# Kernel optimization log

Measured on AMD Instinct MI355X. Metric: run time of the kernel, lower is better.

Reference implementation:

```python
import jax, jax.numpy as jnp
import numpy as np

H = 16      # num_attention_heads
D = 64      # attention_head_size
HID = H * D # hidden_size = 1024
N = 1024    # seq_len == max_len
K = 1024    # position_buckets == att_span (K >= N so un-clamped indices stay in range)
EPS = 1e-7  # layer_norm_eps


def setup_inputs() -> dict:
    key = jax.random.key(0)
    ks = jax.random.split(key, 12)

    def w(k, shape):
        return jax.random.normal(k, shape, dtype=jnp.float32) * 0.02

    return {
        "hidden_states": jax.random.normal(ks[0], (1, N, HID), dtype=jnp.float32),
        "rel_embeddings": jax.random.normal(ks[1], (2 * K, HID), dtype=jnp.float32),
        "Wq": w(ks[2], (HID, HID)), "bq": jnp.zeros((HID,), jnp.float32),
        "Wk": w(ks[3], (HID, HID)), "bk": jnp.zeros((HID,), jnp.float32),
        "Wv": w(ks[4], (HID, HID)), "bv": jnp.zeros((HID,), jnp.float32),
        "Wpk": w(ks[5], (HID, HID)), "bpk": jnp.zeros((HID,), jnp.float32),
        "Wpq": w(ks[6], (HID, HID)), "bpq": jnp.zeros((HID,), jnp.float32),
        "Wo": w(ks[7], (HID, HID)), "bo": jnp.zeros((HID,), jnp.float32),
        "ln_g": jnp.ones((HID,), jnp.float32),
        "ln_b": jnp.zeros((HID,), jnp.float32),
    }


def _heads(x):
    # (L, HID) -> (H, L, D)   (batch size is 1, matching the baked-in id offsets)
    L = x.shape[0]
    return x.reshape(L, H, D).transpose(1, 0, 2)


def reference(hidden_states, rel_embeddings, Wq, bq, Wk, bk, Wv, bv,
              Wpk, bpk, Wpq, bpq, Wo, bo, ln_g, ln_b):
    hs = hidden_states[0]                       # (N, HID)
    q = _heads(hs @ Wq.T + bq)                  # (H, N, D)
    k = _heads(hs @ Wk.T + bk)                  # (H, N, D)
    v = _heads(hs @ Wv.T + bv)                  # (H, N, D)

    scale = jnp.sqrt(jnp.asarray(D * 3, jnp.float32))  # scale_factor = 1 + c2p + p2c = 3
    scores = jnp.einsum('hid,hjd->hij', q, k) / scale  # (H, N, N)

    pos_k = _heads(rel_embeddings @ Wpk.T + bpk)       # (H, 2K, D)
    pos_q = _heads(rel_embeddings @ Wpq.T + bpq)       # (H, 2K, D)

    rows = jnp.arange(N)[:, None]                      # (N, 1)
    # ids[i, j] = (i - j) + K  (no clamp in the original; valid since K >= N)
    idx = K + jnp.arange(N)[:, None] - jnp.arange(N)[None, :]  # (N, N)

    # c2p: gather c2p_att[h, i, K + i - j]
    c2p_att = jnp.einsum('hid,hkd->hik', q, pos_k)     # (H, N, 2K)
    c2p = c2p_att[:, rows, idx]                        # (H, N, N)

    # p2c: gather p2c_att[h, i, K + j - i], then transpose last two dims
    p2c_att = jnp.einsum('hid,hkd->hik', k, pos_q)     # (H, N, 2K)
    p2c = jnp.swapaxes(p2c_att[:, rows, idx.T], -1, -2)  # (H, N, N)

    scores = scores + (c2p + p2c) / scale
    attn = jax.nn.softmax(scores, axis=-1)             # (H, N, N)

    ctx = jnp.einsum('hij,hjd->hid', attn, v)          # (H, N, D)
    ctx = ctx.transpose(1, 0, 2).reshape(1, N, HID)    # (1, N, HID)

    # DebertaV2SelfOutput: dense + residual LayerNorm
    out = ctx @ Wo.T + bo
    x = out + hidden_states
    mu = jnp.mean(x, axis=-1, keepdims=True)
    var = jnp.mean(jnp.square(x - mu), axis=-1, keepdims=True)
    return ((x - mu) / jnp.sqrt(var + EPS)) * ln_g + ln_b
```

## Files before the change

### kernel.cpp

```cpp
#include <hip/hip_runtime.h>
#include <stdint.h>

#define HID 1024
#define NSEQ 1024
#define KREL 1024
#define NHEAD 16
#define DHEAD 64

typedef __attribute__((ext_vector_type(8))) short bhalf8;
typedef __attribute__((ext_vector_type(4))) float floatx4;

__device__ inline uint16_t f2bf(float f) {
  union { float f; uint32_t u; } c; c.f = f;
  uint32_t u = c.u;
  return (uint16_t)((u + 0x7fffu + ((u >> 16) & 1u)) >> 16);
}
__device__ inline uint32_t pkbf(float a, float b) {
  union { float f; uint32_t u; } x, y; x.f = a; y.f = b;
#if __has_builtin(__builtin_amdgcn_perm)
  return __builtin_amdgcn_perm(x.u + 0x8000u, y.u + 0x8000u, 0x03020706u);
#else
  return ((x.u + 0x8000u) >> 16) | ((y.u + 0x8000u) & 0xffff0000u);
#endif
}

struct Cast8 {
  const float* src[8];
  uint16_t* dst[8];
  int n[8];
};
__global__ __launch_bounds__(256) void cast8_kernel(Cast8 c) {
  int seg = blockIdx.y;
  int n = c.n[seg];
  const float* s = c.src[seg];
  uint16_t* d = c.dst[seg];
  for (int idx = (blockIdx.x * 256 + threadIdx.x) * 4; idx < n; idx += 1024 * 256 * 4) {
    float4 v = *(const float4*)(s + idx);
    ushort4 o;
    o.x = f2bf(v.x); o.y = f2bf(v.y); o.z = f2bf(v.z); o.w = f2bf(v.w);
    *(ushort4*)(d + idx) = o;
  }
}

struct ProjArgs {
  const uint16_t* A[5];
  const uint16_t* W[5];
  const float* bias[5];
  uint16_t* C[5];
  int trans[5];
};
__global__ __launch_bounds__(256) void proj_gemm(ProjArgs pa) {
  __shared__ uint16_t a_s[2][128 * 40];
  __shared__ uint16_t b_s[2][128 * 40];
  int bidx = blockIdx.x;
  int xcd = bidx & 7, idx = bidx >> 3;
  int g = xcd * 7 + (idx >> 3);
  int nt = idx & 7;
  int z, mt;
  if (g < 24) { z = g >> 3; mt = g & 7; }
  else { int g2 = g - 24; z = 3 + (g2 >> 4); mt = g2 & 15; }
  const uint16_t* A = pa.A[z];
  const uint16_t* W = pa.W[z];
  int i0 = mt * 128, n0 = nt * 128;

  int t = threadIdx.x;
  int lane = t & 63, w = t >> 6;
  int fm = lane & 15, kq = lane >> 4;
  int wm = (w >> 1) * 64, wn = (w & 1) * 64;

  int ra = t >> 1, ca = (t & 1) * 16;
  const uint16_t* Ap = A + (size_t)(i0 + ra) * HID + ca;
  const uint16_t* Wp = W + (size_t)(n0 + ra) * HID + ca;

  floatx4 acc[4][4] = {};

  uint4 ua0 = *(const uint4*)(Ap);
  uint4 ua1 = *(const uint4*)(Ap + 8);
  uint4 ub0 = *(const uint4*)(Wp);
  uint4 ub1 = *(const uint4*)(Wp + 8);
  *(uint4*)(&a_s[0][ra * 40 + ca]) = ua0;
  *(uint4*)(&a_s[0][ra * 40 + ca + 8]) = ua1;
  *(uint4*)(&b_s[0][ra * 40 + ca]) = ub0;
  *(uint4*)(&b_s[0][ra * 40 + ca + 8]) = ub1;

  for (int kt = 0; kt < 32; ++kt) {
    __syncthreads();
    int cur = kt & 1;
    if (kt < 31) {
      int ko = (kt + 1) * 32;
      ua0 = *(const uint4*)(Ap + ko);
      ua1 = *(const uint4*)(Ap + ko + 8);
      ub0 = *(const uint4*)(Wp + ko);
      ub1 = *(const uint4*)(Wp + ko + 8);
    }
    const uint16_t* as = &a_s[cur][0];
    const uint16_t* bs = &b_s[cur][0];
    bhalf8 af[4], bf[4];
#pragma unroll
    for (int m2 = 0; m2 < 4; ++m2)
      af[m2] = *(bhalf8*)(as + (wm + m2 * 16 + fm) * 40 + kq * 8);
#pragma unroll
    for (int n2 = 0; n2 < 4; ++n2)
      bf[n2] = *(bhalf8*)(bs + (wn + n2 * 16 + fm) * 40 + kq * 8);
#pragma unroll
    for (int m2 = 0; m2 < 4; ++m2)
#pragma unroll
      for (int n2 = 0; n2 < 4; ++n2)
        acc[m2][n2] = __builtin_amdgcn_mfma_f32_16x16x32_bf16(af[m2], bf[n2], acc[m2][n2], 0, 0, 0);
    if (kt < 31) {
      int nxt = cur ^ 1;
      *(uint4*)(&a_s[nxt][ra * 40 + ca]) = ua0;
      *(uint4*)(&a_s[nxt][ra * 40 + ca + 8]) = ua1;
      *(uint4*)(&b_s[nxt][ra * 40 + ca]) = ub0;
      *(uint4*)(&b_s[nxt][ra * 40 + ca + 8]) = ub1;
    }
  }

  const float* bias = pa.bias[z];
  uint16_t* C = pa.C[z];
  int tr = pa.trans[z];
#pragma unroll
  for (int m2 = 0; m2 < 4; ++m2) {
    int rowb = i0 + wm + m2 * 16 + kq * 4;
#pragma unroll
    for (int n2 = 0; n2 < 4; ++n2) {
      int col = n0 + wn + n2 * 16 + fm;
      float bv = bias[col];
      floatx4 v = acc[m2][n2];
      if (tr) {
        uint2 p = { pkbf(v[0] + bv, v[1] + bv), pkbf(v[2] + bv, v[3] + bv) };
        *(uint2*)(C + (size_t)col * NSEQ + rowb) = p;
      } else {
#pragma unroll
        for (int r = 0; r < 4; ++r)
          C[(size_t)(rowb + r) * HID + col] = f2bf(v[r] + bv);
      }
    }
  }
}

__global__ __launch_bounds__(256) void out_gemm(const uint16_t* __restrict__ Abf,
                                                const uint16_t* __restrict__ W,
                                                const float* __restrict__ bias,
                                                float* __restrict__ C) {
  __shared__ uint16_t a_s[2][64 * 40];
  __shared__ uint16_t b_s[2][64 * 40];
  int bidx = blockIdx.x;
  int i0 = (bidx >> 4) * 64, n0 = (bidx & 15) * 64;
  int t = threadIdx.x;
  int lane = t & 63, w = t >> 6;
  int fm = lane & 15, kq = lane >> 4;
  int wm = (w >> 1) * 32, wn = (w & 1) * 32;
  int ra = t >> 2, ca = (t & 3) * 8;
  const uint16_t* Ap = Abf + (size_t)(i0 + ra) * HID + ca;
  const uint16_t* Wp = W + (size_t)(n0 + ra) * HID + ca;
  floatx4 acc00 = {0,0,0,0}, acc01 = {0,0,0,0}, acc10 = {0,0,0,0}, acc11 = {0,0,0,0};
  uint4 ua = *(const uint4*)(Ap);
  uint4 ub = *(const uint4*)(Wp);
  *(uint4*)(&a_s[0][ra * 40 + ca]) = ua;
  *(uint4*)(&b_s[0][ra * 40 + ca]) = ub;
  for (int kt = 0; kt < 32; ++kt) {
    __syncthreads();
    int cur = kt & 1;
    if (kt < 31) {
      int ko = (kt + 1) * 32;
      ua = *(const uint4*)(Ap + ko);
      ub = *(const uint4*)(Wp + ko);
    }
    const uint16_t* as = &a_s[cur][0];
    const uint16_t* bs = &b_s[cur][0];
    bhalf8 a0 = *(bhalf8*)(as + (wm + fm) * 40 + kq * 8);
    bhalf8 a1 = *(bhalf8*)(as + (wm + 16 + fm) * 40 + kq * 8);
    bhalf8 b0 = *(bhalf8*)(bs + (wn + fm) * 40 + kq * 8);
    bhalf8 b1 = *(bhalf8*)(bs + (wn + 16 + fm) * 40 + kq * 8);
    acc00 = __builtin_amdgcn_mfma_f32_16x16x32_bf16(a0, b0, acc00, 0, 0, 0);
    acc01 = __builtin_amdgcn_mfma_f32_16x16x32_bf16(a0, b1, acc01, 0, 0, 0);
    acc10 = __builtin_amdgcn_mfma_f32_16x16x32_bf16(a1, b0, acc10, 0, 0, 0);
    acc11 = __builtin_amdgcn_mfma_f32_16x16x32_bf16(a1, b1, acc11, 0, 0, 0);
    if (kt < 31) {
      int nxt = cur ^ 1;
      *(uint4*)(&a_s[nxt][ra * 40 + ca]) = ua;
      *(uint4*)(&b_s[nxt][ra * 40 + ca]) = ub;
    }
  }
  int rb0 = kq * 4;
#define EPO(ACC, SM, SN)                                                   \
  {                                                                        \
    int rowb = i0 + wm + (SM)*16 + rb0;                                    \
    int col = n0 + wn + (SN)*16 + fm;                                      \
    float bv_ = bias[col];                                                 \
    _Pragma("unroll")                                                      \
    for (int rr = 0; rr < 4; ++rr)                                         \
      C[(size_t)(rowb + rr) * HID + col] = ACC[rr] + bv_;                  \
  }
  EPO(acc00, 0, 0) EPO(acc01, 0, 1) EPO(acc10, 1, 0) EPO(acc11, 1, 1)
#undef EPO
}

__global__ __launch_bounds__(256) void attn_kernel(const uint16_t* __restrict__ qg,
                                                   const uint16_t* __restrict__ kg,
                                                   const uint16_t* __restrict__ vtg,
                                                   const uint16_t* __restrict__ pkg,
                                                   const uint16_t* __restrict__ pqg,
                                                   uint16_t* __restrict__ ctx) {
  const float RSCALE = 0.07216878364870323f;
  __shared__ uint16_t Qs[32][72];
  __shared__ uint16_t Ks[32][72];
  __shared__ uint16_t Vt[64][40];
  __shared__ float C2Ps[2][32][68];
  __shared__ float P2C[2][32][68];
  __shared__ float Sqk[2][32][36];
  __shared__ uint16_t Pbf[32][40];
  __shared__ float m_sm[32], l_sm[32], al_sm[32];

  int t = threadIdx.x;
  int lane = t & 63, w = t >> 6;
  int fm = lane & 15;
  int kq = lane >> 4;

  int b = blockIdx.x;
  int xcd = b & 7, slot = b >> 3;
  int h = xcd * 2 + (slot & 1);
  int i0 = (slot >> 1) * 32;
  int cb = h * DHEAD;

  {
    int r = t >> 3, chq = (t & 7) * 8;
    *(uint4*)(&Qs[r][chq]) = *(const uint4*)(qg + (size_t)(i0 + r) * HID + cb + chq);
  }
  if (t < 32) { m_sm[t] = -1e30f; l_sm[t] = 0.f; }

  floatx4 opv0 = {0,0,0,0}, opv1 = {0,0,0,0};
  int wn = w * 16;
  int smt = w >> 1, snt = w & 1;
  int i2 = t >> 3, jj4 = (t & 7) * 4;

  int pr = t >> 3, pch = (t & 7) * 8;
  int rV = t >> 2, cV = (t & 3) * 8;
  const uint16_t* kb = kg + cb + pch;
  const uint16_t* vb = vtg + (size_t)(cb + rV) * HID + cV;

  int ntb = (w & 1) * 2;
  int brow_f = ntb * 16 + fm;
  const uint16_t* bgp = ((w < 2) ? pkg : pqg) + cb + kq * 8;
  int cbase = 31 - brow_f + kq * 4;

  uint4 rk, rv;
  bhalf8 nbA0, nbA1, nbB0, nbB1;

#define STAGE1(BUF, BA0, BA1, BB0, BB1)                                          \
  do {                                                                           \
    if (w < 2) {                                                                 \
      _Pragma("unroll")                                                          \
      for (int mt = 0; mt < 2; ++mt) {                                           \
        bhalf8 a0 = *(bhalf8*)(&Qs[mt * 16 + fm][kq * 8]);                       \
        bhalf8 a1 = *(bhalf8*)(&Qs[mt * 16 + fm][kq * 8 + 32]);                  \
        floatx4 ac0 = {0,0,0,0}, ac1 = {0,0,0,0};                                \
        ac0 = __builtin_amdgcn_mfma_f32_16x16x32_bf16(a0, BA0, ac0, 0, 0, 0);    \
        ac0 = __builtin_amdgcn_mfma_f32_16x16x32_bf16(a1, BA1, ac0, 0, 0, 0);    \
        ac1 = __builtin_amdgcn_mfma_f32_16x16x32_bf16(a0, BB0, ac1, 0, 0, 0);    \
        ac1 = __builtin_amdgcn_mfma_f32_16x16x32_bf16(a1, BB1, ac1, 0, 0, 0);    \
        _Pragma("unroll")                                                        \
        for (int r = 0; r < 4; ++r) {                                            \
          int i = mt * 16 + kq * 4 + r;                                          \
          C2Ps[BUF][i][(cbase + mt * 16 + r) & 63] = ac0[r];                     \
          C2Ps[BUF][i][(cbase + mt * 16 + r - 16) & 63] = ac1[r];                \
        }                                                                        \
      }                                                                          \
    } else {                                                                     \
      _Pragma("unroll")                                                          \
      for (int mt = 0; mt < 2; ++mt) {                                           \
        bhalf8 a0 = *(bhalf8*)(&Ks[mt * 16 + fm][kq * 8]);                       \
        bhalf8 a1 = *(bhalf8*)(&Ks[mt * 16 + fm][kq * 8 + 32]);                  \
        floatx4 ac0 = {0,0,0,0}, ac1 = {0,0,0,0};                                \
        ac0 = __builtin_amdgcn_mfma_f32_16x16x32_bf16(a0, BA0, ac0, 0, 0, 0);    \
        ac0 = __builtin_amdgcn_mfma_f32_16x16x32_bf16(a1, BA1, ac0, 0, 0, 0);    \
        ac1 = __builtin_amdgcn_mfma_f32_16x16x32_bf16(a0, BB0, ac1, 0, 0, 0);    \
        ac1 = __builtin_amdgcn_mfma_f32_16x16x32_bf16(a1, BB1, ac1, 0, 0, 0);    \
        _Pragma("unroll")                                                        \
        for (int r = 0; r < 4; ++r) {                                            \
          int jr = mt * 16 + kq * 4 + r;                                         \
          P2C[BUF][jr][brow_f] = ac0[r];                                         \
          P2C[BUF][jr][brow_f + 16] = ac1[r];                                    \
        }                                                                        \
      }                                                                          \
    }                                                                            \
    {                                                                            \
      bhalf8 qa0 = *(bhalf8*)(&Qs[smt * 16 + fm][kq * 8]);                       \
      bhalf8 qa1 = *(bhalf8*)(&Qs[smt * 16 + fm][kq * 8 + 32]);                  \
      bhalf8 kb0 = *(bhalf8*)(&Ks[snt * 16 + fm][kq * 8]);                       \
      bhalf8 kb1 = *(bhalf8*)(&Ks[snt * 16 + fm][kq * 8 + 32]);                  \
      floatx4 sacc = {0,0,0,0};                                                  \
      sacc = __builtin_amdgcn_mfma_f32_16x16x32_bf16(qa0, kb0, sacc, 0, 0, 0);   \
      sacc = __builtin_amdgcn_mfma_f32_16x16x32_bf16(qa1, kb1, sacc, 0, 0, 0);   \
      _Pragma("unroll")                                                          \
      for (int r = 0; r < 4; ++r)                                                \
        Sqk[BUF][smt * 16 + kq * 4 + r][snt * 16 + fm] = sacc[r];                \
    }                                                                            \
  } while (0)

  rk = *(const uint4*)(kb);
  rv = *(const uint4*)(vb);
  *(uint4*)(&Ks[pr][pch]) = rk;
  *(uint4*)(&Vt[rV][cV]) = rv;
  __syncthreads();
  rk = *(const uint4*)(kb + (size_t)(32 + pr) * HID);
  rv = *(const uint4*)(vb + 32);
  {
    int rbase = KREL + i0 - 31;
    int r0 = rbase + brow_f;      if (r0 > 2047) r0 = 2047;
    int r1 = rbase + brow_f + 16; if (r1 > 2047) r1 = 2047;
    bhalf8 tA0 = *(const bhalf8*)(bgp + ((size_t)r0 << 10));
    bhalf8 tA1 = *(const bhalf8*)(bgp + ((size_t)r0 << 10) + 32);
    bhalf8 tB0 = *(const bhalf8*)(bgp + ((size_t)r1 << 10));
    bhalf8 tB1 = *(const bhalf8*)(bgp + ((size_t)r1 << 10) + 32);
    STAGE1(0, tA0, tA1, tB0, tB1);
  }
  __syncthreads();
  {
    *(uint4*)(&Ks[pr][pch]) = rk;
    rk = *(const uint4*)(kb + (size_t)(64 + pr) * HID);
    int rb1 = KREL + i0 - 63;
    int r0 = rb1 + brow_f;
    nbA0 = *(const bhalf8*)(bgp + ((size_t)r0 << 10));
    nbA1 = *(const bhalf8*)(bgp + ((size_t)r0 << 10) + 32);
    nbB0 = *(const bhalf8*)(bgp + ((size_t)(r0 + 16) << 10));
    nbB1 = *(const bhalf8*)(bgp + ((size_t)(r0 + 16) << 10) + 32);
  }
  __syncthreads();

  for (int jt = 0; jt < NSEQ / 32; ++jt) {
    int cur = jt & 1;

    float4 v_sqk = *(const float4*)(&Sqk[cur][i2][jj4]);
    float4 v_c2p = *(const float4*)(&C2Ps[cur][i2][jj4]);
    float p0 = P2C[cur][jj4 + 0][i2 - jj4 + 31];
    float p1 = P2C[cur][jj4 + 1][i2 - jj4 + 30];
    float p2 = P2C[cur][jj4 + 2][i2 - jj4 + 29];
    float p3 = P2C[cur][jj4 + 3][i2 - jj4 + 28];

    if (jt < 31) {
      int bi = cur ^ 1;
      STAGE1(bi, nbA0, nbA1, nbB0, nbB1);
    }

    {
      float sv0 = (v_sqk.x + v_c2p.x + p0) * RSCALE;
      float sv1 = (v_sqk.y + v_c2p.y + p1) * RSCALE;
      float sv2 = (v_sqk.z + v_c2p.z + p2) * RSCALE;
      float sv3 = (v_sqk.w + v_c2p.w + p3) * RSCALE;
      float mx = fmaxf(fmaxf(sv0, sv1), fmaxf(sv2, sv3));
      mx = fmaxf(mx, __shfl_xor(mx, 1));
      mx = fmaxf(mx, __shfl_xor(mx, 2));
      mx = fmaxf(mx, __shfl_xor(mx, 4));
      float m_old = m_sm[i2];
      float m_new = fmaxf(m_old, mx);
      float al = __expf(m_old - m_new);
      float e0 = __expf(sv0 - m_new);
      float e1 = __expf(sv1 - m_new);
      float e2 = __expf(sv2 - m_new);
      float e3 = __expf(sv3 - m_new);
      uint2 pk2v;
      pk2v.x = (uint32_t)f2bf(e0) | ((uint32_t)f2bf(e1) << 16);
      pk2v.y = (uint32_t)f2bf(e2) | ((uint32_t)f2bf(e3) << 16);
      *(uint2*)(&Pbf[i2][jj4]) = pk2v;
      float ts = (e0 + e1) + (e2 + e3);
      ts += __shfl_xor(ts, 1);
      ts += __shfl_xor(ts, 2);
      ts += __shfl_xor(ts, 4);
      if (jj4 == 0) { m_sm[i2] = m_new; l_sm[i2] = l_sm[i2] * al + ts; al_sm[i2] = al; }
    }
    __syncthreads();

    {
      floatx4 al0 = *(const floatx4*)(&al_sm[kq * 4]);
      floatx4 al1 = *(const floatx4*)(&al_sm[16 + kq * 4]);
#pragma unroll
      for (int r = 0; r < 4; ++r) {
        opv0[r] *= al0[r];
        opv1[r] *= al1[r];
      }
      bhalf8 vbf = *(bhalf8*)(&Vt[wn + fm][kq * 8]);
      bhalf8 pa0 = *(bhalf8*)(&Pbf[fm][kq * 8]);
      bhalf8 pa1 = *(bhalf8*)(&Pbf[16 + fm][kq * 8]);
      opv0 = __builtin_amdgcn_mfma_f32_16x16x32_bf16(pa0, vbf, opv0, 0, 0, 0);
      opv1 = __builtin_amdgcn_mfma_f32_16x16x32_bf16(pa1, vbf, opv1, 0, 0, 0);
      if (jt < 31) *(uint4*)(&Vt[rV][cV]) = rv;
      if (jt < 30) rv = *(const uint4*)(vb + (jt + 2) * 32);
    }
    if (jt < 30) {
      *(uint4*)(&Ks[pr][pch]) = rk;
    }
    if (jt < 29) {
      rk = *(const uint4*)(kb + (size_t)((jt + 3) * 32 + pr) * HID);
    }
    if (jt < 30) {
      int rb = KREL + i0 - (jt + 2) * 32 - 31;
      int r0 = rb + brow_f;
      nbA0 = *(const bhalf8*)(bgp + ((size_t)r0 << 10));
      nbA1 = *(const bhalf8*)(bgp + ((size_t)r0 << 10) + 32);
      nbB0 = *(const bhalf8*)(bgp + ((size_t)(r0 + 16) << 10));
      nbB1 = *(const bhalf8*)(bgp + ((size_t)(r0 + 16) << 10) + 32);
    }
    __syncthreads();
  }
#undef STAGE1

  {
    floatx4 l0 = *(const floatx4*)(&l_sm[kq * 4]);
    floatx4 l1 = *(const floatx4*)(&l_sm[16 + kq * 4]);
#pragma unroll
    for (int r = 0; r < 4; ++r) {
      int ia = kq * 4 + r, ib = 16 + kq * 4 + r;
      ctx[(size_t)(i0 + ia) * HID + cb + wn + fm] = f2bf(opv0[r] / l0[r]);
      ctx[(size_t)(i0 + ib) * HID + cb + wn + fm] = f2bf(opv1[r] / l1[r]);
    }
  }
}

__global__ __launch_bounds__(256) void ln_kernel(const float* __restrict__ xin,
                                                 const float* __restrict__ hs,
                                                 const float* __restrict__ g,
                                                 const float* __restrict__ b,
                                                 float* __restrict__ y) {
  int row = blockIdx.x, t = threadIdx.x;
  int c = t * 4;
  float4 a = *(const float4*)(xin + (size_t)row * HID + c);
  float4 hv = *(const float4*)(hs + (size_t)row * HID + c);
  float x0 = a.x + hv.x, x1 = a.y + hv.y, x2 = a.z + hv.z, x3 = a.w + hv.w;
  float s = x0 + x1 + x2 + x3;
  float sq = x0 * x0 + x1 * x1 + x2 * x2 + x3 * x3;
  for (int off = 32; off; off >>= 1) {
    s += __shfl_xor(s, off);
    sq += __shfl_xor(sq, off);
  }
  __shared__ float rs[4], rq[4];
  int w = t >> 6, lane = t & 63;
  if (lane == 0) { rs[w] = s; rq[w] = sq; }
  __syncthreads();
  s = rs[0] + rs[1] + rs[2] + rs[3];
  sq = rq[0] + rq[1] + rq[2] + rq[3];
  float mu = s * (1.0f / HID);
  float var = sq * (1.0f / HID) - mu * mu;
  float rstd = rsqrtf(var + 1e-7f);
  float4 gg = *(const float4*)(g + c);
  float4 bb = *(const float4*)(b + c);
  float4 out;
  out.x = (x0 - mu) * rstd * gg.x + bb.x;
  out.y = (x1 - mu) * rstd * gg.y + bb.y;
  out.z = (x2 - mu) * rstd * gg.z + bb.z;
  out.w = (x3 - mu) * rstd * gg.w + bb.w;
  *(float4*)(y + (size_t)row * HID + c) = out;
}

extern "C" void kernel_launch(void* const* d_in, const int* in_sizes, int n_in,
                              void* d_out, int out_size, void* d_ws, size_t ws_size,
                              hipStream_t stream) {
  const float* hs  = (const float*)d_in[0];
  const float* rel = (const float*)d_in[1];
  const float* Wq  = (const float*)d_in[2];  const float* bq  = (const float*)d_in[3];
  const float* Wk  = (const float*)d_in[4];  const float* bk  = (const float*)d_in[5];
  const float* Wv  = (const float*)d_in[6];  const float* bv  = (const float*)d_in[7];
  const float* Wpk = (const float*)d_in[8];  const float* bpk = (const float*)d_in[9];
  const float* Wpq = (const float*)d_in[10]; const float* bpq = (const float*)d_in[11];
  const float* Wo  = (const float*)d_in[12]; const float* bo  = (const float*)d_in[13];
  const float* lng = (const float*)d_in[14]; const float* lnb = (const float*)d_in[15];

  char* ws = (char*)d_ws;
  const size_t MB = 1024 * 1024;
  uint16_t* q_bf   = (uint16_t*)(ws + 0 * MB);
  uint16_t* k_bf   = (uint16_t*)(ws + 2 * MB);
  uint16_t* vt_bf  = (uint16_t*)(ws + 4 * MB);
  uint16_t* pk_bf  = (uint16_t*)(ws + 6 * MB);
  uint16_t* pq_bf  = (uint16_t*)(ws + 10 * MB);
  uint16_t* ctx_bf = (uint16_t*)(ws + 14 * MB);
  float*    out_f  = (float*)   (ws + 16 * MB);
  uint16_t* hs_bf  = (uint16_t*)(ws + 20 * MB);
  uint16_t* rel_bf = (uint16_t*)(ws + 22 * MB);
  uint16_t* Wq_bf  = (uint16_t*)(ws + 26 * MB);
  uint16_t* Wk_bf  = (uint16_t*)(ws + 28 * MB);
  uint16_t* Wv_bf  = (uint16_t*)(ws + 30 * MB);
  uint16_t* Wpk_bf = (uint16_t*)(ws + 32 * MB);
  uint16_t* Wpq_bf = (uint16_t*)(ws + 34 * MB);
  uint16_t* Wo_bf  = (uint16_t*)(ws + 36 * MB);

  dim3 blk(256);

  Cast8 c8;
  c8.src[0] = hs;  c8.dst[0] = hs_bf;  c8.n[0] = 1024 * 1024;
  c8.src[1] = rel; c8.dst[1] = rel_bf; c8.n[1] = 2048 * 1024;
  c8.src[2] = Wq;  c8.dst[2] = Wq_bf;  c8.n[2] = 1024 * 1024;
  c8.src[3] = Wk;  c8.dst[3] = Wk_bf;  c8.n[3] = 1024 * 1024;
  c8.src[4] = Wv;  c8.dst[4] = Wv_bf;  c8.n[4] = 1024 * 1024;
  c8.src[5] = Wpk; c8.dst[5] = Wpk_bf; c8.n[5] = 1024 * 1024;
  c8.src[6] = Wpq; c8.dst[6] = Wpq_bf; c8.n[6] = 1024 * 1024;
  c8.src[7] = Wo;  c8.dst[7] = Wo_bf;  c8.n[7] = 1024 * 1024;
  cast8_kernel<<<dim3(1024, 8), blk, 0, stream>>>(c8);

  ProjArgs pa;
  pa.A[0] = hs_bf;  pa.A[1] = hs_bf;  pa.A[2] = hs_bf;  pa.A[3] = rel_bf; pa.A[4] = rel_bf;
  pa.W[0] = Wq_bf;  pa.W[1] = Wk_bf;  pa.W[2] = Wv_bf;  pa.W[3] = Wpk_bf; pa.W[4] = Wpq_bf;
  pa.bias[0] = bq;  pa.bias[1] = bk;  pa.bias[2] = bv;  pa.bias[3] = bpk; pa.bias[4] = bpq;
  pa.C[0] = q_bf; pa.C[1] = k_bf; pa.C[2] = vt_bf; pa.C[3] = pk_bf; pa.C[4] = pq_bf;
  pa.trans[0] = 0; pa.trans[1] = 0; pa.trans[2] = 1; pa.trans[3] = 0; pa.trans[4] = 0;
  proj_gemm<<<dim3(448), blk, 0, stream>>>(pa);

  attn_kernel<<<dim3(512), blk, 0, stream>>>(q_bf, k_bf, vt_bf, pk_bf, pq_bf, ctx_bf);

  out_gemm<<<dim3(256), blk, 0, stream>>>(ctx_bf, Wo_bf, bo, out_f);

  ln_kernel<<<dim3(1024), blk, 0, stream>>>(out_f, hs, lng, lnb, (float*)d_out);
}
```

Baseline: 200.4 us.

## Fuse residual LayerNorm into output GEMM via atomic row stats and last-block finalize

The out_gemm epilogue now adds bias and the residual, writes the pre-norm rows, and accumulates per-row sum and sum-of-squares with atomics. The last of the 16 column blocks in each 64-row band then applies LayerNorm for that band, which removes the separate ln_kernel launch. The stats buffer reuses the hs_bf workspace region and is zeroed by block 0 of attn_kernel, after proj_gemm has finished reading hs_bf. The cost is float atomics, a serialized tail where a single block normalizes 64 rows, and non-deterministic summation order.

```diff
diff --git a/kernel.cpp b/kernel.cpp
--- a/kernel.cpp
+++ b/kernel.cpp
@@ -142,7 +142,12 @@
 __global__ __launch_bounds__(256) void out_gemm(const uint16_t* __restrict__ Abf,
                                                 const uint16_t* __restrict__ W,
                                                 const float* __restrict__ bias,
-                                                float* __restrict__ C) {
+                                                const float* __restrict__ hsf,
+                                                const float* __restrict__ gvec,
+                                                const float* __restrict__ bvec,
+                                                float* __restrict__ outf,
+                                                float* __restrict__ stats,
+                                                float* __restrict__ dout) {
   __shared__ uint16_t a_s[2][64 * 40];
   __shared__ uint16_t b_s[2][64 * 40];
   int bidx = blockIdx.x;
@@ -183,18 +188,61 @@
       *(uint4*)(&b_s[nxt][ra * 40 + ca]) = ub;
     }
   }
-  int rb0 = kq * 4;
-#define EPO(ACC, SM, SN)                                                   \
-  {                                                                        \
-    int rowb = i0 + wm + (SM)*16 + rb0;                                    \
-    int col = n0 + wn + (SN)*16 + fm;                                      \
-    float bv_ = bias[col];                                                 \
-    _Pragma("unroll")                                                      \
-    for (int rr = 0; rr < 4; ++rr)                                         \
-      C[(size_t)(rowb + rr) * HID + col] = ACC[rr] + bv_;                  \
-  }
-  EPO(acc00, 0, 0) EPO(acc01, 0, 1) EPO(acc10, 1, 0) EPO(acc11, 1, 1)
-#undef EPO
+
+  float* rsum = stats;
+  float* rsq = stats + 1024;
+  uint32_t* cnt = (uint32_t*)(stats + 2048);
+  int band = bidx >> 4;
+
+#define EPO2(ACC0, ACC1, SM)                                                   \
+  {                                                                            \
+    _Pragma("unroll")                                                          \
+    for (int rr = 0; rr < 4; ++rr) {                                           \
+      int row = i0 + wm + (SM)*16 + kq * 4 + rr;                               \
+      int c0 = n0 + wn + fm, c1 = c0 + 16;                                     \
+      float x0 = ACC0[rr] + bias[c0] + hsf[(size_t)row * HID + c0];            \
+      float x1 = ACC1[rr] + bias[c1] + hsf[(size_t)row * HID + c1];            \
+      outf[(size_t)row * HID + c0] = x0;                                       \
+      outf[(size_t)row * HID + c1] = x1;                                       \
+      float s_ = x0 + x1, q_ = x0 * x0 + x1 * x1;                              \
+      s_ += __shfl_xor(s_, 1); q_ += __shfl_xor(q_, 1);                        \
+      s_ += __shfl_xor(s_, 2); q_ += __shfl_xor(q_, 2);                        \
+      s_ += __shfl_xor(s_, 4); q_ += __shfl_xor(q_, 4);                        \
+      s_ += __shfl_xor(s_, 8); q_ += __shfl_xor(q_, 8);                        \
+      if ((lane & 15) == 0) {                                                  \
+        atomicAdd(&rsum[row], s_);                                             \
+        atomicAdd(&rsq[row], q_);                                              \
+      }                                                                        \
+    }                                                                          \
+  }
+  EPO2(acc00, acc01, 0)
+  EPO2(acc10, acc11, 1)
+#undef EPO2
+
+  __threadfence();
+  __shared__ int lastf;
+  __syncthreads();
+  if (t == 0) lastf = (atomicAdd(&cnt[band], 1u) == 15u);
+  __syncthreads();
+  if (!lastf) return;
+  __threadfence();
+
+  int c = t * 4;
+  float4 gg = *(const float4*)(gvec + c);
+  float4 bb = *(const float4*)(bvec + c);
+  for (int r = 0; r < 64; ++r) {
+    int row = i0 + r;
+    float mu = rsum[row] * (1.0f / HID);
+    float var = rsq[row] * (1.0f / HID) - mu * mu;
+    float rstd = rsqrtf(var + 1e-7f);
+    float4 x = *(const float4*)(outf + (size_t)row * HID + c);
+    float4 o;
+    o.x = (x.x - mu) * rstd * gg.x + bb.x;
+    o.y = (x.y - mu) * rstd * gg.y + bb.y;
+    o.z = (x.z - mu) * rstd * gg.z + bb.z;
+    o.w = (x.w - mu) * rstd * gg.w + bb.w;
+    *(float4*)(dout + (size_t)row * HID + c) = o;
+  }
 }
 
 __global__ __launch_bounds__(256) void attn_kernel(const uint16_t* __restrict__ qg,
@@ -202,7 +250,8 @@
                                                    const uint16_t* __restrict__ vtg,
                                                    const uint16_t* __restrict__ pkg,
                                                    const uint16_t* __restrict__ pqg,
-                                                   uint16_t* __restrict__ ctx) {
+                                                   uint16_t* __restrict__ ctx,
+                                                   float* __restrict__ stats) {
   const float RSCALE = 0.07216878364870323f;
   __shared__ uint16_t Qs[32][72];
   __shared__ uint16_t Ks[32][72];
@@ -219,6 +268,10 @@
   int kq = lane >> 4;
 
   int b = blockIdx.x;
+  if (b == 0) {
+    for (int i = t; i < 2048; i += 256) stats[i] = 0.f;
+    if (t < 16) ((uint32_t*)(stats + 2048))[t] = 0u;
+  }
   int xcd = b & 7, slot = b >> 3;
   int h = xcd * 2 + (slot & 1);
   int i0 = (slot >> 1) * 32;
@@ -418,41 +471,6 @@
   }
 }
 
-__global__ __launch_bounds__(256) void ln_kernel(const float* __restrict__ xin,
-                                                 const float* __restrict__ hs,
-                                                 const float* __restrict__ g,
-                                                 const float* __restrict__ b,
-                                                 float* __restrict__ y) {
-  int row = blockIdx.x, t = threadIdx.x;
-  int c = t * 4;
-  float4 a = *(const float4*)(xin + (size_t)row * HID + c);
-  float4 hv = *(const float4*)(hs + (size_t)row * HID + c);
-  float x0 = a.x + hv.x, x1 = a.y + hv.y, x2 = a.z + hv.z, x3 = a.w + hv.w;
-  float s = x0 + x1 + x2 + x3;
-  float sq = x0 * x0 + x1 * x1 + x2 * x2 + x3 * x3;
-  for (int off = 32; off; off >>= 1) {
-    s += __shfl_xor(s, off);
-    sq += __shfl_xor(sq, off);
-  }
-  __shared__ float rs[4], rq[4];
-  int w = t >> 6, lane = t & 63;
-  if (lane == 0) { rs[w] = s; rq[w] = sq; }
-  __syncthreads();
-  s = rs[0] + rs[1] + rs[2] + rs[3];
-  sq = rq[0] + rq[1] + rq[2] + rq[3];
-  float mu = s * (1.0f / HID);
-  float var = sq * (1.0f / HID) - mu * mu;
-  float rstd = rsqrtf(var + 1e-7f);
-  float4 gg = *(const float4*)(g + c);
-  float4 bb = *(const float4*)(b + c);
-  float4 out;
-  out.x = (x0 - mu) * rstd * gg.x + bb.x;
-  out.y = (x1 - mu) * rstd * gg.y + bb.y;
-  out.z = (x2 - mu) * rstd * gg.z + bb.z;
-  out.w = (x3 - mu) * rstd * gg.w + bb.w;
-  *(float4*)(y + (size_t)row * HID + c) = out;
-}
-
 extern "C" void kernel_launch(void* const* d_in, const int* in_sizes, int n_in,
                               void* d_out, int out_size, void* d_ws, size_t ws_size,
                               hipStream_t stream) {
@@ -483,6 +501,7 @@
   uint16_t* Wpk_bf = (uint16_t*)(ws + 32 * MB);
   uint16_t* Wpq_bf = (uint16_t*)(ws + 34 * MB);
   uint16_t* Wo_bf  = (uint16_t*)(ws + 36 * MB);
+  float*    stats  = (float*)   (ws + 20 * MB);
 
   dim3 blk(256);
 
@@ -505,9 +524,8 @@
   pa.trans[0] = 0; pa.trans[1] = 0; pa.trans[2] = 1; pa.trans[3] = 0; pa.trans[4] = 0;
   proj_gemm<<<dim3(448), blk, 0, stream>>>(pa);
 
-  attn_kernel<<<dim3(512), blk, 0, stream>>>(q_bf, k_bf, vt_bf, pk_bf, pq_bf, ctx_bf);
-
-  out_gemm<<<dim3(256), blk, 0, stream>>>(ctx_bf, Wo_bf, bo, out_f);
-
-  ln_kernel<<<dim3(1024), blk, 0, stream>>>(out_f, hs, lng, lnb, (float*)d_out);
-}
+  attn_kernel<<<dim3(512), blk, 0, stream>>>(q_bf, k_bf, vt_bf, pk_bf, pq_bf, ctx_bf, stats);
+
+  out_gemm<<<dim3(256), blk, 0, stream>>>(ctx_bf, Wo_bf, bo, hs, lng, lnb, out_f, stats,
+                                          (float*)d_out);
+}
```

Result: slower. 239.5 us (+19.5%).
